# Performance work log

Hardware: AMD Instinct MI355X
Metric: run time of the kernel (lower is better)

The kernel has to match this reference:

```python
import jax, jax.numpy as jnp
import numpy as np

B, S, H, NH = 8, 1024, 768, 12
DK = H // NH  # 64


def setup_inputs() -> dict:
    key = jax.random.key(0)
    ks = jax.random.split(key, 7)
    sc = 0.02
    return {
        "Q": jax.random.normal(ks[0], (B, S, H), jnp.float32),
        "K": jax.random.normal(ks[1], (B, S, H), jnp.float32),
        "V": jax.random.normal(ks[2], (B, S, H), jnp.float32),
        "Wq": jax.random.normal(ks[3], (H, H), jnp.float32) * sc,
        "Wk": jax.random.normal(ks[4], (H, H), jnp.float32) * sc,
        "Wv": jax.random.normal(ks[5], (H, H), jnp.float32) * sc,
        "Wo": jax.random.normal(ks[6], (H, H), jnp.float32) * sc,
    }


def reference(Q, K, V, Wq, Wk, Wv, Wo):
    # torch Linear(bias=False): y = x @ W.T, weight shape [out, in]
    q = jnp.einsum('bsh,oh->bso', Q, Wq).reshape(B, S, NH, DK)
    k = jnp.einsum('bsh,oh->bso', K, Wk).reshape(B, S, NH, DK)
    v = jnp.einsum('bsh,oh->bso', V, Wv).reshape(B, S, NH, DK)
    # naive SDPA per head: full [B,NH,S,S] score matrix, scale by sqrt(dk)
    scores = jnp.einsum('bqnd,bknd->bnqk', q, k) / jnp.sqrt(jnp.float32(DK))
    w = jax.nn.softmax(scores, axis=-1)
    c = jnp.einsum('bnqk,bknd->bqnd', w, v).reshape(B, S, H)
    return jnp.einsum('bsh,oh->bso', c, Wo)
```

## Files before the change

kernel.cpp:

```cpp
#include <hip/hip_runtime.h>
#include <hip/hip_bf16.h>

#define B_   8
#define S_   1024
#define H_   768
#define NH_  12
#define DK_  64
#define M_   (B_ * S_)

typedef __attribute__((ext_vector_type(8))) short          short8;
typedef __attribute__((ext_vector_type(8))) unsigned short ushort8;
typedef __attribute__((ext_vector_type(4))) unsigned short ushort4v;
typedef __attribute__((ext_vector_type(4))) float          f32x4;

__device__ __forceinline__ unsigned short f2bf(float x) {
    union { __hip_bfloat16 h; unsigned short u; } r;
    r.h = __float2bfloat16(x);
    return r.u;
}

__device__ __forceinline__ unsigned cvtpk_bf16(float lo, float hi) {
    unsigned r;
    asm("v_cvt_pk_bf16_f32 %0, %1, %2" : "=v"(r) : "v"(lo), "v"(hi));
    return r;
}

__global__ __launch_bounds__(256)
void cvt_w(const float* __restrict__ w0, const float* __restrict__ w1,
           const float* __restrict__ w2, const float* __restrict__ w3,
           unsigned short* __restrict__ o0, unsigned short* __restrict__ o1,
           unsigned short* __restrict__ o2, unsigned short* __restrict__ o3)
{
    const int wsel = blockIdx.y;
    const float* src = (wsel == 0) ? w0 : (wsel == 1) ? w1 : (wsel == 2) ? w2 : w3;
    unsigned short* dst = (wsel == 0) ? o0 : (wsel == 1) ? o1 : (wsel == 2) ? o2 : o3;
    const float s = (wsel == 0) ? 0.125f * 1.44269504089f : 1.0f;
    const int i = blockIdx.x * 256 + threadIdx.x;
    const float4 x = ((const float4*)src)[i];
    ushort4v o;
    o[0] = f2bf(x.x * s); o[1] = f2bf(x.y * s);
    o[2] = f2bf(x.z * s); o[3] = f2bf(x.w * s);
    ((ushort4v*)dst)[i] = o;
}

template<bool A_BF16, bool OUT_BF16>
__global__ __launch_bounds__(256)
void gemm_bt(const void* __restrict__ A0, const void* __restrict__ A1,
             const void* __restrict__ A2,
             const unsigned short* __restrict__ W0,
             const unsigned short* __restrict__ W1,
             const unsigned short* __restrict__ W2,
             void* __restrict__ C0, void* __restrict__ C1, void* __restrict__ C2)
{
    __shared__ unsigned short As[128 * 32];
    __shared__ unsigned short Bs[128 * 32];

    const int tid  = threadIdx.x;
    const int z    = blockIdx.z;
    const int bm   = blockIdx.x, bn = blockIdx.y;
    const int w    = tid >> 6, lane = tid & 63;
    const int lg   = lane >> 4, lc = lane & 15;
    const int wm   = (w >> 1) * 64, wn = (w & 1) * 64;

    const void* Av = (z == 0) ? A0 : (z == 1) ? A1 : A2;
    const unsigned short* Bw = (z == 0) ? W0 : (z == 1) ? W1 : W2;
    void* Cv = (z == 0) ? C0 : (z == 1) ? C1 : C2;

    const float*          Af = (const float*)Av;
    const unsigned short* Ah = (const unsigned short*)Av;

    f32x4 acc[4][4] = {};

    for (int k0 = 0; k0 < H_; k0 += 32) {
        if (A_BF16) {
#pragma unroll
            for (int i = 0; i < 2; i++) {
                const int gI = i * 256 + tid;
                const int row = gI >> 2, c8 = (gI & 3) * 8;
                *(ushort8*)&As[row * 32 + c8] =
                    *(const ushort8*)&Ah[(size_t)(bm * 128 + row) * H_ + k0 + c8];
            }
        } else {
#pragma unroll
            for (int i = 0; i < 4; i++) {
                const int gI = i * 256 + tid;
                const int row = gI >> 3, c4 = (gI & 7) * 4;
                const float4 x = *(const float4*)&Af[(size_t)(bm * 128 + row) * H_ + k0 + c4];
                ushort4v o4;
                o4[0] = f2bf(x.x); o4[1] = f2bf(x.y);
                o4[2] = f2bf(x.z); o4[3] = f2bf(x.w);
                *(ushort4v*)&As[row * 32 + c4] = o4;
            }
        }
#pragma unroll
        for (int i = 0; i < 2; i++) {
            const int gI = i * 256 + tid;
            const int row = gI >> 2, c8 = (gI & 3) * 8;
            *(ushort8*)&Bs[row * 32 + c8] =
                *(const ushort8*)&Bw[(size_t)(bn * 128 + row) * H_ + k0 + c8];
        }
        __syncthreads();

        short8 af[4], bfr[4];
#pragma unroll
        for (int mi = 0; mi < 4; mi++)
            af[mi] = *(const short8*)&As[(wm + mi * 16 + lc) * 32 + lg * 8];
#pragma unroll
        for (int ni = 0; ni < 4; ni++)
            bfr[ni] = *(const short8*)&Bs[(wn + ni * 16 + lc) * 32 + lg * 8];
#pragma unroll
        for (int mi = 0; mi < 4; mi++)
#pragma unroll
            for (int ni = 0; ni < 4; ni++)
                acc[mi][ni] = __builtin_amdgcn_mfma_f32_16x16x32_bf16(
                    af[mi], bfr[ni], acc[mi][ni], 0, 0, 0);
        __syncthreads();
    }

#pragma unroll
    for (int mi = 0; mi < 4; mi++)
#pragma unroll
        for (int ni = 0; ni < 4; ni++)
#pragma unroll
            for (int reg = 0; reg < 4; reg++) {
                const int row = bm * 128 + wm + mi * 16 + lg * 4 + reg;
                const int col = bn * 128 + wn + ni * 16 + lc;
                if (OUT_BF16)
                    ((unsigned short*)Cv)[(size_t)row * H_ + col] = f2bf(acc[mi][ni][reg]);
                else
                    ((float*)Cv)[(size_t)row * H_ + col] = acc[mi][ni][reg];
            }
}

__global__ __launch_bounds__(256)
void attn(const unsigned short* __restrict__ q,
          const unsigned short* __restrict__ k,
          const unsigned short* __restrict__ v,
          unsigned short* __restrict__ c)
{
    __shared__ unsigned short Ks[2][64][72];
    __shared__ unsigned short Vt[2][64][72];

    const int tid  = threadIdx.x;
    const int qt   = blockIdx.x, h = blockIdx.y, b = blockIdx.z;
    const int wid  = tid >> 6;
    const int lane = tid & 63;
    const int lg   = lane >> 4, lc = lane & 15;
    const int r    = tid >> 2;
    const int d0   = (tid & 3) * 16;
    const int g    = tid & 3;
    const size_t base = (size_t)b * S_ * H_ + (size_t)h * DK_;
    const int colv = r ^ (g << 4);

    short8 aq[2][2];
#pragma unroll
    for (int m = 0; m < 2; m++)
#pragma unroll
        for (int ks = 0; ks < 2; ks++)
            aq[m][ks] = *(const short8*)
                &q[base + (size_t)(qt * 128 + wid * 32 + m * 16 + lc) * H_ + ks * 32 + lg * 8];

    f32x4 o[2][4] = {};
    float mrow[2] = {-1e30f, -1e30f}, lrow[2] = {0.f, 0.f};

    const int NT = S_ / 64;

    ushort8 kr0, kr1, vr0, vr1;
    {
        const unsigned short* ksrc = &k[base + (size_t)r * H_ + d0];
        const unsigned short* vsrc = &v[base + (size_t)r * H_ + d0];
        kr0 = *(const ushort8*)ksrc; kr1 = *(const ushort8*)(ksrc + 8);
        vr0 = *(const ushort8*)vsrc; vr1 = *(const ushort8*)(vsrc + 8);
    }
    *(ushort8*)&Ks[0][r][d0]     = kr0;
    *(ushort8*)&Ks[0][r][d0 + 8] = kr1;
#pragma unroll
    for (int j = 0; j < 8; j++) Vt[0][d0 + j][colv]     = vr0[j];
#pragma unroll
    for (int j = 0; j < 8; j++) Vt[0][d0 + 8 + j][colv] = vr1[j];
    __syncthreads();

    int cur = 0;
    for (int kt = 0; kt < NT; kt++) {
        const bool more = (kt + 1 < NT);
        if (more) {
            const unsigned short* ksrc = &k[base + (size_t)((kt + 1) * 64 + r) * H_ + d0];
            const unsigned short* vsrc = &v[base + (size_t)((kt + 1) * 64 + r) * H_ + d0];
            kr0 = *(const ushort8*)ksrc; kr1 = *(const ushort8*)(ksrc + 8);
            vr0 = *(const ushort8*)vsrc; vr1 = *(const ushort8*)(vsrc + 8);
        }

        f32x4 st[2][4] = {};
        __builtin_amdgcn_s_setprio(1);
#pragma unroll
        for (int ni = 0; ni < 4; ni++)
#pragma unroll
            for (int ks = 0; ks < 2; ks++) {
                const short8 bk = *(const short8*)&Ks[cur][ni * 16 + lc][ks * 32 + lg * 8];
                st[0][ni] = __builtin_amdgcn_mfma_f32_16x16x32_bf16(bk, aq[0][ks], st[0][ni], 0, 0, 0);
                st[1][ni] = __builtin_amdgcn_mfma_f32_16x16x32_bf16(bk, aq[1][ks], st[1][ni], 0, 0, 0);
            }
        __builtin_amdgcn_s_setprio(0);

        unsigned pw[2][4][2];
        float pmax[2];
#pragma unroll
        for (int m = 0; m < 2; m++) {
            float pm = st[m][0][0];
#pragma unroll
            for (int ni = 0; ni < 4; ni++)
#pragma unroll
                for (int reg = 0; reg < 4; reg++)
                    pm = fmaxf(pm, st[m][ni][reg]);
            pm = fmaxf(pm, __shfl_xor(pm, 16, 64));
            pm = fmaxf(pm, __shfl_xor(pm, 32, 64));
            pmax[m] = pm;
        }

        if (__any((pmax[0] > mrow[0] + 8.f) | (pmax[1] > mrow[1] + 8.f))) {
#pragma unroll
            for (int m = 0; m < 2; m++) {
                const float mnew  = fmaxf(mrow[m], pmax[m]);
                const float scale = exp2f(mrow[m] - mnew);
                lrow[m] *= scale;
                mrow[m]  = mnew;
                float scr[4];
#pragma unroll
                for (int reg = 0; reg < 4; reg++)
                    scr[reg] = __shfl(scale, lg * 4 + reg, 64);
#pragma unroll
                for (int ni = 0; ni < 4; ni++)
#pragma unroll
                    for (int reg = 0; reg < 4; reg++)
                        o[m][ni][reg] *= scr[reg];
            }
        }

#pragma unroll
        for (int m = 0; m < 2; m++) {
            float psum = 0.f;
#pragma unroll
            for (int ni = 0; ni < 4; ni++)
#pragma unroll
                for (int reg = 0; reg < 4; reg++) {
                    const float p = exp2f(st[m][ni][reg] - mrow[m]);
                    st[m][ni][reg] = p; psum += p;
                }
            psum += __shfl_xor(psum, 16, 64);
            psum += __shfl_xor(psum, 32, 64);
            lrow[m] += psum;
#pragma unroll
            for (int ni = 0; ni < 4; ni++) {
                pw[m][ni][0] = cvtpk_bf16(st[m][ni][0], st[m][ni][1]);
                pw[m][ni][1] = cvtpk_bf16(st[m][ni][2], st[m][ni][3]);
            }
        }

        const int sl0 = lc + ((lg & 1) << 5);
        const int sl1 = sl0 + 16;
        const bool hi = (lg >> 1) != 0;
        short8 pa[2][2];
#pragma unroll
        for (int m = 0; m < 2; m++)
#pragma unroll
            for (int ks = 0; ks < 2; ks++) {
                const unsigned lo0 = pw[m][2 * ks][0],     lo1 = pw[m][2 * ks][1];
                const unsigned hi0 = pw[m][2 * ks + 1][0], hi1 = pw[m][2 * ks + 1][1];
                union { unsigned u[4]; short8 s8; } pk;
                const unsigned a0l = __shfl(lo0, sl0, 64), a0h = __shfl(hi0, sl0, 64);
                const unsigned a1l = __shfl(lo1, sl0, 64), a1h = __shfl(hi1, sl0, 64);
                const unsigned a2l = __shfl(lo0, sl1, 64), a2h = __shfl(hi0, sl1, 64);
                const unsigned a3l = __shfl(lo1, sl1, 64), a3h = __shfl(hi1, sl1, 64);
                pk.u[0] = hi ? a0h : a0l;
                pk.u[1] = hi ? a1h : a1l;
                pk.u[2] = hi ? a2h : a2l;
                pk.u[3] = hi ? a3h : a3l;
                pa[m][ks] = pk.s8;
            }

        __builtin_amdgcn_s_setprio(1);
#pragma unroll
        for (int ni = 0; ni < 4; ni++)
#pragma unroll
            for (int ks = 0; ks < 2; ks++) {
                const short8 bv = *(const short8*)
                    &Vt[cur][ni * 16 + lc][(ks * 32 + lg * 8) ^ (ni << 4)];
                o[0][ni] = __builtin_amdgcn_mfma_f32_16x16x32_bf16(pa[0][ks], bv, o[0][ni], 0, 0, 0);
                o[1][ni] = __builtin_amdgcn_mfma_f32_16x16x32_bf16(pa[1][ks], bv, o[1][ni], 0, 0, 0);
            }
        __builtin_amdgcn_s_setprio(0);

        if (more) {
            *(ushort8*)&Ks[cur ^ 1][r][d0]     = kr0;
            *(ushort8*)&Ks[cur ^ 1][r][d0 + 8] = kr1;
#pragma unroll
            for (int j = 0; j < 8; j++) Vt[cur ^ 1][d0 + j][colv]     = vr0[j];
#pragma unroll
            for (int j = 0; j < 8; j++) Vt[cur ^ 1][d0 + 8 + j][colv] = vr1[j];
        }
        __syncthreads();
        cur ^= 1;
    }

#pragma unroll
    for (int m = 0; m < 2; m++) {
        const float iv = 1.0f / lrow[m];
#pragma unroll
        for (int reg = 0; reg < 4; reg++) {
            const float ivr = __shfl(iv, lg * 4 + reg, 64);
            const int row = qt * 128 + wid * 32 + m * 16 + lg * 4 + reg;
#pragma unroll
            for (int ni = 0; ni < 4; ni++)
                c[base + (size_t)row * H_ + ni * 16 + lc] = f2bf(o[m][ni][reg] * ivr);
        }
    }
}

extern "C" void kernel_launch(void* const* d_in, const int* in_sizes, int n_in,
                              void* d_out, int out_size, void* d_ws, size_t ws_size,
                              hipStream_t stream)
{
    const float* Q  = (const float*)d_in[0];
    const float* K  = (const float*)d_in[1];
    const float* V  = (const float*)d_in[2];
    const float* Wq = (const float*)d_in[3];
    const float* Wk = (const float*)d_in[4];
    const float* Wv = (const float*)d_in[5];
    const float* Wo = (const float*)d_in[6];

    unsigned short* qb = (unsigned short*)d_ws;
    unsigned short* kb = qb + (size_t)M_ * H_;
    unsigned short* vb = kb + (size_t)M_ * H_;
    unsigned short* cb = vb + (size_t)M_ * H_;
    unsigned short* wq = cb + (size_t)M_ * H_;
    unsigned short* wk = wq + (size_t)H_ * H_;
    unsigned short* wv = wk + (size_t)H_ * H_;
    unsigned short* wo = wv + (size_t)H_ * H_;

    cvt_w<<<dim3(H_ * H_ / 4 / 256, 4), 256, 0, stream>>>(
        Wq, Wk, Wv, Wo, wq, wk, wv, wo);

    gemm_bt<false, true><<<dim3(M_ / 128, H_ / 128, 3), 256, 0, stream>>>(
        Q, K, V, wq, wk, wv, qb, kb, vb);

    attn<<<dim3(S_ / 128, NH_, B_), 256, 0, stream>>>(qb, kb, vb, cb);

    gemm_bt<true, false><<<dim3(M_ / 128, H_ / 128, 1), 256, 0, stream>>>(
        cb, cb, cb, wo, wo, wo, d_out, d_out, d_out);
}
```

Baseline: 150.7 us.

## Pre-transpose V globally and load K/V fragments directly from global memory

Adds a separate kernel that writes V transposed per (batch, head) into a new workspace buffer. The attention kernel drops its LDS double-buffering and block barriers and instead loads K and V^T MFMA fragments straight from global memory into registers. It also remaps the grid to 1D so that blocks sharing a (b,h) pair are spread apart, and it reuses V's buffer for the context output. The aim is to remove the LDS staging, the scatter-transpose and the syncthreads from the hot loop. In exchange it adds a kernel launch and extra global traffic, and every wave now re-reads K/V from L2 with global-load latency that is no longer hidden by the prefetch.

```diff
diff --git a/kernel.cpp b/kernel.cpp
--- a/kernel.cpp
+++ b/kernel.cpp
@@ -133,24 +133,51 @@
 }
 
 __global__ __launch_bounds__(256)
+void transpose_v(const unsigned short* __restrict__ v,
+                 unsigned short* __restrict__ vt)
+{
+    __shared__ unsigned short T[64][72];
+    const int tid = threadIdx.x;
+    const int st0 = blockIdx.x, h = blockIdx.y, b = blockIdx.z;
+    const int r = tid >> 2, d0 = (tid & 3) * 16, g = tid & 3;
+
+    const unsigned short* src = &v[(size_t)(b * S_ + st0 * 64 + r) * H_ + h * DK_ + d0];
+    const ushort8 v0 = *(const ushort8*)src;
+    const ushort8 v1 = *(const ushort8*)(src + 8);
+    const int colv = r ^ (g << 4);
+#pragma unroll
+    for (int j = 0; j < 8; j++) T[d0 + j][colv]     = v0[j];
+#pragma unroll
+    for (int j = 0; j < 8; j++) T[d0 + 8 + j][colv] = v1[j];
+    __syncthreads();
+
+    const size_t ob = ((size_t)(b * NH_ + h) * DK_) * S_ + st0 * 64;
+#pragma unroll
+    for (int half = 0; half < 2; half++) {
+        const int ci = half * 256 + tid;
+        const int d = ci >> 3, kc = ci & 7;
+        const int sw = ((d >> 4) & 3) << 4;
+        const ushort8 val = *(const ushort8*)&T[d][(kc * 8) ^ sw];
+        *(ushort8*)&vt[ob + (size_t)d * S_ + kc * 8] = val;
+    }
+}
+
+__global__ __launch_bounds__(256)
 void attn(const unsigned short* __restrict__ q,
           const unsigned short* __restrict__ k,
-          const unsigned short* __restrict__ v,
+          const unsigned short* __restrict__ vt,
           unsigned short* __restrict__ c)
 {
-    __shared__ unsigned short Ks[2][64][72];
-    __shared__ unsigned short Vt[2][64][72];
-
     const int tid  = threadIdx.x;
-    const int qt   = blockIdx.x, h = blockIdx.y, b = blockIdx.z;
+    const int dlin = blockIdx.x;
+    const int p    = dlin % 96;
+    const int qt   = dlin / 96;
+    const int b    = p / NH_, h = p % NH_;
     const int wid  = tid >> 6;
     const int lane = tid & 63;
     const int lg   = lane >> 4, lc = lane & 15;
-    const int r    = tid >> 2;
-    const int d0   = (tid & 3) * 16;
-    const int g    = tid & 3;
     const size_t base = (size_t)b * S_ * H_ + (size_t)h * DK_;
-    const int colv = r ^ (g << 4);
+    const size_t vtb  = (size_t)(b * NH_ + h) * DK_ * S_;
 
     short8 aq[2][2];
 #pragma unroll
@@ -163,32 +190,14 @@
     f32x4 o[2][4] = {};
     float mrow[2] = {-1e30f, -1e30f}, lrow[2] = {0.f, 0.f};
 
-    const int NT = S_ / 64;
-
-    ushort8 kr0, kr1, vr0, vr1;
-    {
-        const unsigned short* ksrc = &k[base + (size_t)r * H_ + d0];
-        const unsigned short* vsrc = &v[base + (size_t)r * H_ + d0];
-        kr0 = *(const ushort8*)ksrc; kr1 = *(const ushort8*)(ksrc + 8);
-        vr0 = *(const ushort8*)vsrc; vr1 = *(const ushort8*)(vsrc + 8);
-    }
-    *(ushort8*)&Ks[0][r][d0]     = kr0;
-    *(ushort8*)&Ks[0][r][d0 + 8] = kr1;
-#pragma unroll
-    for (int j = 0; j < 8; j++) Vt[0][d0 + j][colv]     = vr0[j];
-#pragma unroll
-    for (int j = 0; j < 8; j++) Vt[0][d0 + 8 + j][colv] = vr1[j];
-    __syncthreads();
-
-    int cur = 0;
-    for (int kt = 0; kt < NT; kt++) {
-        const bool more = (kt + 1 < NT);
-        if (more) {
-            const unsigned short* ksrc = &k[base + (size_t)((kt + 1) * 64 + r) * H_ + d0];
-            const unsigned short* vsrc = &v[base + (size_t)((kt + 1) * 64 + r) * H_ + d0];
-            kr0 = *(const ushort8*)ksrc; kr1 = *(const ushort8*)(ksrc + 8);
-            vr0 = *(const ushort8*)vsrc; vr1 = *(const ushort8*)(vsrc + 8);
-        }
+    for (int kt = 0; kt < S_ / 64; kt++) {
+        short8 bk[4][2];
+#pragma unroll
+        for (int ni = 0; ni < 4; ni++)
+#pragma unroll
+            for (int ks = 0; ks < 2; ks++)
+                bk[ni][ks] = *(const short8*)
+                    &k[base + (size_t)(kt * 64 + ni * 16 + lc) * H_ + ks * 32 + lg * 8];
 
         f32x4 st[2][4] = {};
         __builtin_amdgcn_s_setprio(1);
@@ -196,11 +205,18 @@
         for (int ni = 0; ni < 4; ni++)
 #pragma unroll
             for (int ks = 0; ks < 2; ks++) {
-                const short8 bk = *(const short8*)&Ks[cur][ni * 16 + lc][ks * 32 + lg * 8];
-                st[0][ni] = __builtin_amdgcn_mfma_f32_16x16x32_bf16(bk, aq[0][ks], st[0][ni], 0, 0, 0);
-                st[1][ni] = __builtin_amdgcn_mfma_f32_16x16x32_bf16(bk, aq[1][ks], st[1][ni], 0, 0, 0);
+                st[0][ni] = __builtin_amdgcn_mfma_f32_16x16x32_bf16(bk[ni][ks], aq[0][ks], st[0][ni], 0, 0, 0);
+                st[1][ni] = __builtin_amdgcn_mfma_f32_16x16x32_bf16(bk[ni][ks], aq[1][ks], st[1][ni], 0, 0, 0);
             }
         __builtin_amdgcn_s_setprio(0);
+
+        short8 bv[4][2];
+#pragma unroll
+        for (int ni = 0; ni < 4; ni++)
+#pragma unroll
+            for (int ks = 0; ks < 2; ks++)
+                bv[ni][ks] = *(const short8*)
+                    &vt[vtb + (size_t)(ni * 16 + lc) * S_ + kt * 64 + ks * 32 + lg * 8];
 
         unsigned pw[2][4][2];
         float pmax[2];
@@ -243,8 +259,8 @@
             for (int ni = 0; ni < 4; ni++)
 #pragma unroll
                 for (int reg = 0; reg < 4; reg++) {
-                    const float p = exp2f(st[m][ni][reg] - mrow[m]);
-                    st[m][ni][reg] = p; psum += p;
+                    const float pp = exp2f(st[m][ni][reg] - mrow[m]);
+                    st[m][ni][reg] = pp; psum += pp;
                 }
             psum += __shfl_xor(psum, 16, 64);
             psum += __shfl_xor(psum, 32, 64);
@@ -283,23 +299,10 @@
         for (int ni = 0; ni < 4; ni++)
 #pragma unroll
             for (int ks = 0; ks < 2; ks++) {
-                const short8 bv = *(const short8*)
-                    &Vt[cur][ni * 16 + lc][(ks * 32 + lg * 8) ^ (ni << 4)];
-                o[0][ni] = __builtin_amdgcn_mfma_f32_16x16x32_bf16(pa[0][ks], bv, o[0][ni], 0, 0, 0);
-                o[1][ni] = __builtin_amdgcn_mfma_f32_16x16x32_bf16(pa[1][ks], bv, o[1][ni], 0, 0, 0);
+                o[0][ni] = __builtin_amdgcn_mfma_f32_16x16x32_bf16(pa[0][ks], bv[ni][ks], o[0][ni], 0, 0, 0);
+                o[1][ni] = __builtin_amdgcn_mfma_f32_16x16x32_bf16(pa[1][ks], bv[ni][ks], o[1][ni], 0, 0, 0);
             }
         __builtin_amdgcn_s_setprio(0);
-
-        if (more) {
-            *(ushort8*)&Ks[cur ^ 1][r][d0]     = kr0;
-            *(ushort8*)&Ks[cur ^ 1][r][d0 + 8] = kr1;
-#pragma unroll
-            for (int j = 0; j < 8; j++) Vt[cur ^ 1][d0 + j][colv]     = vr0[j];
-#pragma unroll
-            for (int j = 0; j < 8; j++) Vt[cur ^ 1][d0 + 8 + j][colv] = vr1[j];
-        }
-        __syncthreads();
-        cur ^= 1;
     }
 
 #pragma unroll
@@ -331,8 +334,9 @@
     unsigned short* qb = (unsigned short*)d_ws;
     unsigned short* kb = qb + (size_t)M_ * H_;
     unsigned short* vb = kb + (size_t)M_ * H_;
-    unsigned short* cb = vb + (size_t)M_ * H_;
-    unsigned short* wq = cb + (size_t)M_ * H_;
+    unsigned short* vtb = vb + (size_t)M_ * H_;
+    unsigned short* cb  = vb;
+    unsigned short* wq = vtb + (size_t)M_ * H_;
     unsigned short* wk = wq + (size_t)H_ * H_;
     unsigned short* wv = wk + (size_t)H_ * H_;
     unsigned short* wo = wv + (size_t)H_ * H_;
@@ -343,7 +347,9 @@
     gemm_bt<false, true><<<dim3(M_ / 128, H_ / 128, 3), 256, 0, stream>>>(
         Q, K, V, wq, wk, wv, qb, kb, vb);
 
-    attn<<<dim3(S_ / 128, NH_, B_), 256, 0, stream>>>(qb, kb, vb, cb);
+    transpose_v<<<dim3(S_ / 64, NH_, B_), 256, 0, stream>>>(vb, vtb);
+
+    attn<<<dim3(768), 256, 0, stream>>>(qb, kb, vtb, cb);
 
     gemm_bt<true, false><<<dim3(M_ / 128, H_ / 128, 1), 256, 0, stream>>>(
         cb, cb, cb, wo, wo, wo, d_out, d_out, d_out);
```

After: 178.8 us. 18.7% more time.
